# Kernel optimization log

Measured on AMD Instinct MI355X. Metric: run time of the kernel, lower is better.

Reference implementation:

```python
import jax, jax.numpy as jnp
import numpy as np

V, D = 1000000, 128
B, K = 4096, 50


def setup_inputs() -> dict:
    key = jax.random.key(0)
    k1, k2, k3, k4 = jax.random.split(key, 4)
    return {
        "emb_batch": jax.random.normal(k1, (B, D), dtype=jnp.float32),
        "embedding": jax.random.normal(k2, (V, D), dtype=jnp.float32),
        "attr_sim": jax.random.uniform(k3, (B, K), dtype=jnp.float32),
        "indices": jax.random.randint(k4, (B, K), 0, V),
        "beta": 1,
    }


def reference(emb_batch, embedding, attr_sim, indices, beta):
    # gather per-sample neighbor embeddings: [B, K, D]
    gathered = embedding[indices]
    # squared L2 distance to each sample's own embedding: [B, K]
    sq = jnp.sum((gathered - emb_batch[:, None, :]) ** 2, axis=-1)
    # per-sample weighted sum with attr_sim, then mean over batch (scalar)
    return jnp.sum(sq * attr_sim) / emb_batch.shape[0]
```

## Files before the change

kernel.cpp:

```cpp
#include <hip/hip_runtime.h>

#define B_N 4096
#define K_N 50
#define D_N 128
#define WAVES_PER_BLOCK 4
#define BLOCK_T 256
#define NBLOCKS (B_N / WAVES_PER_BLOCK)

__global__ __launch_bounds__(BLOCK_T) void disloss_main(
    const float* __restrict__ emb_batch,
    const float* __restrict__ embedding,
    const float* __restrict__ attr_sim,
    const int*   __restrict__ indices,
    float*       __restrict__ partials)
{
    const int wave = threadIdx.x >> 6;
    const int lane = threadIdx.x & 63;
    const int b = blockIdx.x * WAVES_PER_BLOCK + wave;

    const float2 eb = *reinterpret_cast<const float2*>(&emb_batch[(size_t)b * D_N + lane * 2]);

    int   myidx  = 0;
    float myattr = 0.0f;
    if (lane < K_N) {
        myidx  = indices[(size_t)b * K_N + lane];
        myattr = attr_sim[(size_t)b * K_N + lane];
    }

    float acc = 0.0f;
    #pragma unroll 10
    for (int k = 0; k < K_N; ++k) {
        const int   idx = __shfl(myidx,  k);
        const float a   = __shfl(myattr, k);
        const float2 g = *reinterpret_cast<const float2*>(
            &embedding[(size_t)idx * D_N + lane * 2]);
        const float dx = g.x - eb.x;
        const float dy = g.y - eb.y;
        acc += a * (dx * dx + dy * dy);
    }

    #pragma unroll
    for (int off = 32; off > 0; off >>= 1)
        acc += __shfl_down(acc, off);

    __shared__ float s[WAVES_PER_BLOCK];
    if (lane == 0) s[wave] = acc;
    __syncthreads();
    if (threadIdx.x == 0)
        partials[blockIdx.x] = s[0] + s[1] + s[2] + s[3];
}

__global__ __launch_bounds__(BLOCK_T) void disloss_reduce(
    const float* __restrict__ partials,
    float*       __restrict__ out)
{
    float acc = 0.0f;
    for (int i = threadIdx.x; i < NBLOCKS; i += BLOCK_T)
        acc += partials[i];

    #pragma unroll
    for (int off = 32; off > 0; off >>= 1)
        acc += __shfl_down(acc, off);

    __shared__ float s[WAVES_PER_BLOCK];
    const int wave = threadIdx.x >> 6;
    const int lane = threadIdx.x & 63;
    if (lane == 0) s[wave] = acc;
    __syncthreads();
    if (threadIdx.x == 0)
        out[0] = (s[0] + s[1] + s[2] + s[3]) / (float)B_N;
}

extern "C" void kernel_launch(void* const* d_in, const int* in_sizes, int n_in,
                              void* d_out, int out_size, void* d_ws, size_t ws_size,
                              hipStream_t stream) {
    const float* emb_batch = (const float*)d_in[0];
    const float* embedding = (const float*)d_in[1];
    const float* attr_sim  = (const float*)d_in[2];
    const int*   indices   = (const int*)d_in[3];

    float* out      = (float*)d_out;
    float* partials = (float*)d_ws;

    disloss_main<<<NBLOCKS, BLOCK_T, 0, stream>>>(emb_batch, embedding, attr_sim,
                                                  indices, partials);
    disloss_reduce<<<1, BLOCK_T, 0, stream>>>(partials, out);
}
```

Baseline: 24.14 us.

## Split each sample across two waves with half-wave float4 row gathers

```diff
diff --git a/kernel.cpp b/kernel.cpp
--- a/kernel.cpp
+++ b/kernel.cpp
@@ -3,9 +3,10 @@
 #define B_N 4096
 #define K_N 50
 #define D_N 128
+#define BLOCK_T 256
 #define WAVES_PER_BLOCK 4
-#define BLOCK_T 256
-#define NBLOCKS (B_N / WAVES_PER_BLOCK)
+#define SAMPLES_PER_BLOCK 2
+#define NBLOCKS (B_N / SAMPLES_PER_BLOCK)
 
 __global__ __launch_bounds__(BLOCK_T) void disloss_main(
     const float* __restrict__ emb_batch,
@@ -16,38 +17,49 @@
 {
     const int wave = threadIdx.x >> 6;
     const int lane = threadIdx.x & 63;
-    const int b = blockIdx.x * WAVES_PER_BLOCK + wave;
+    const int half = lane >> 5;
+    const int sub  = (lane & 31) * 4;
+    const int s    = wave >> 1;
+    const int p    = wave & 1;
+    const int b    = blockIdx.x * SAMPLES_PER_BLOCK + s;
 
-    const float2 eb = *reinterpret_cast<const float2*>(&emb_batch[(size_t)b * D_N + lane * 2]);
+    const float4 eb = *reinterpret_cast<const float4*>(
+        &emb_batch[(size_t)b * D_N + sub]);
+
+    const int kbase  = p ? 26 : 0;
+    const int npairs = p ? 12 : 13;
 
     int   myidx  = 0;
     float myattr = 0.0f;
-    if (lane < K_N) {
-        myidx  = indices[(size_t)b * K_N + lane];
-        myattr = attr_sim[(size_t)b * K_N + lane];
+    if (lane < 2 * npairs) {
+        myidx  = indices[(size_t)b * K_N + kbase + lane];
+        myattr = attr_sim[(size_t)b * K_N + kbase + lane];
     }
 
     float acc = 0.0f;
-    #pragma unroll 10
-    for (int k = 0; k < K_N; ++k) {
-        const int   idx = __shfl(myidx,  k);
-        const float a   = __shfl(myattr, k);
-        const float2 g = *reinterpret_cast<const float2*>(
-            &embedding[(size_t)idx * D_N + lane * 2]);
+    #pragma unroll 4
+    for (int it = 0; it < npairs; ++it) {
+        const int   kl  = 2 * it + half;
+        const int   idx = __shfl(myidx,  kl);
+        const float a   = __shfl(myattr, kl);
+        const float4 g = *reinterpret_cast<const float4*>(
+            &embedding[(size_t)idx * D_N + sub]);
         const float dx = g.x - eb.x;
         const float dy = g.y - eb.y;
-        acc += a * (dx * dx + dy * dy);
+        const float dz = g.z - eb.z;
+        const float dw = g.w - eb.w;
+        acc += a * (dx * dx + dy * dy + dz * dz + dw * dw);
     }
 
     #pragma unroll
     for (int off = 32; off > 0; off >>= 1)
         acc += __shfl_down(acc, off);
 
-    __shared__ float s[WAVES_PER_BLOCK];
-    if (lane == 0) s[wave] = acc;
+    __shared__ float smem[WAVES_PER_BLOCK];
+    if (lane == 0) smem[wave] = acc;
     __syncthreads();
     if (threadIdx.x == 0)
-        partials[blockIdx.x] = s[0] + s[1] + s[2] + s[3];
+        partials[blockIdx.x] = smem[0] + smem[1] + smem[2] + smem[3];
 }
 
 __global__ __launch_bounds__(BLOCK_T) void disloss_reduce(
@@ -55,6 +67,7 @@
     float*       __restrict__ out)
 {
     float acc = 0.0f;
+    #pragma unroll
     for (int i = threadIdx.x; i < NBLOCKS; i += BLOCK_T)
         acc += partials[i];
 
@@ -62,13 +75,13 @@
     for (int off = 32; off > 0; off >>= 1)
         acc += __shfl_down(acc, off);
 
-    __shared__ float s[WAVES_PER_BLOCK];
+    __shared__ float smem[WAVES_PER_BLOCK];
     const int wave = threadIdx.x >> 6;
     const int lane = threadIdx.x & 63;
-    if (lane == 0) s[wave] = acc;
+    if (lane == 0) smem[wave] = acc;
     __syncthreads();
     if (threadIdx.x == 0)
-        out[0] = (s[0] + s[1] + s[2] + s[3]) / (float)B_N;
+        out[0] = (smem[0] + smem[1] + smem[2] + smem[3]) / (float)B_N;
 }
 
 extern "C" void kernel_launch(void* const* d_in, const int* in_sizes, int n_in,
```

Measured after the change: 24.29 us. Within noise of the previous version (+0.6%).
